# Performance work log

Measured on AMD Instinct MI355X. Metric: run time of the kernel, lower is better.

The kernel has to match this reference:

```python
import jax, jax.numpy as jnp
import numpy as np

N_NODES = 100000
N_EDGES = 1600000
N_GRAPHS = 1000
H = 128
F_IN = 128
F_EDGE = 16
DEPTH = 4


def setup_inputs() -> dict:
    key = jax.random.key(0)
    ks = jax.random.split(key, 10)
    s = 1.0 / np.sqrt(H)
    x = jax.random.normal(ks[0], (N_NODES, F_IN), dtype=jnp.float32)
    edge_index = jax.random.randint(ks[1], (2, N_EDGES), 0, N_NODES, dtype=jnp.int32)
    edge_attr = jax.random.normal(ks[2], (N_EDGES, F_EDGE), dtype=jnp.float32)
    batch = jnp.sort(jax.random.randint(ks[3], (N_NODES,), 0, N_GRAPHS, dtype=jnp.int32))
    W0 = jax.random.normal(ks[4], (F_IN, H), dtype=jnp.float32) * s
    b0 = jnp.zeros((H,), dtype=jnp.float32)
    W1 = jax.random.normal(ks[5], (DEPTH, H, H), dtype=jnp.float32) * s
    b1 = jnp.zeros((DEPTH, H), dtype=jnp.float32)
    W2 = jax.random.normal(ks[6], (DEPTH, H, H), dtype=jnp.float32) * s
    b2 = jnp.zeros((DEPTH, H), dtype=jnp.float32)
    Wf = jax.random.normal(ks[7], (H, 1), dtype=jnp.float32) * s
    bf = jnp.zeros((1,), dtype=jnp.float32)
    return {"x": x, "edge_index": edge_index, "edge_attr": edge_attr, "batch": batch,
            "W0": W0, "b0": b0, "W1": W1, "b1": b1, "W2": W2, "b2": b2, "Wf": Wf, "bf": bf}


def reference(x, edge_index, edge_attr, batch, W0, b0, W1, b1, W2, b2, Wf, bf):
    # edge_attr is read by the original forward but never used in the math.
    src, dst = edge_index[0], edge_index[1]
    n = x.shape[0]
    h0 = jax.nn.relu(x @ W0 + b0)  # [N, H]
    h = h0
    for i in range(DEPTH):
        # GINConv (eps=0): MLP(x + sum_{j in N(i)} x_j); messages flow src -> dst
        agg = jax.ops.segment_sum(h[src], dst, num_segments=n)  # [N, H]
        z = h + agg
        z = jax.nn.relu(z @ W1[i] + b1[i]) @ W2[i] + b2[i]
        # residual then relu (dropout p=0.02 is identity at eval)
        h = jax.nn.relu(z + h0)
    pooled = jax.ops.segment_sum(h, batch, num_segments=N_GRAPHS)  # [G, H]
    out = (pooled @ Wf + bf)[:, 0]  # [G]
    return out
```

## Files before the change

kernel.cpp:

```cpp
#include <hip/hip_runtime.h>

#define N_NODES 100000
#define N_EDGES 1600000
#define N_GRAPHS 1000
#define H 128
#define DEPTH 4
#define NB 391
#define BCAP 4864

typedef __attribute__((ext_vector_type(8))) short bf16x8;
typedef __attribute__((ext_vector_type(4))) float f32x4;

__device__ __forceinline__ unsigned short f2bf(float f) {
  unsigned int u = __float_as_uint(f);
  u += 0x7FFF + ((u >> 16) & 1);
  return (unsigned short)(u >> 16);
}
__device__ __forceinline__ float bflo(unsigned int v) { return __uint_as_float(v << 16); }
__device__ __forceinline__ float bfhi(unsigned int v) { return __uint_as_float(v & 0xFFFF0000u); }

__global__ __launch_bounds__(256) void k_bcnt(const int* __restrict__ dst, int* __restrict__ gcnt) {
  __shared__ int c[NB];
  int tid = threadIdx.x, e0 = blockIdx.x * 4096;
  for (int i = tid; i < NB; i += 256) c[i] = 0;
  __syncthreads();
#pragma unroll
  for (int i = 0; i < 16; ++i) {
    int e = e0 + i * 256 + tid;
    if (e < N_EDGES) atomicAdd(&c[dst[e] >> 8], 1);
  }
  __syncthreads();
  for (int i = tid; i < NB; i += 256)
    if (c[i]) atomicAdd(&gcnt[i], c[i]);
}

__global__ __launch_bounds__(512) void k_bscan(const int* __restrict__ gcnt, int* __restrict__ boff,
                                               int* __restrict__ cursor) {
  __shared__ int sh[512];
  int t = threadIdx.x;
  int v = (t < NB) ? gcnt[t] : 0;
  sh[t] = v;
  __syncthreads();
  for (int s = 1; s < 512; s <<= 1) {
    int x = (t >= s) ? sh[t - s] : 0;
    __syncthreads();
    sh[t] += x;
    __syncthreads();
  }
  if (t < NB) {
    int e = sh[t] - v;
    boff[t] = e;
    cursor[t] = e;
  }
  if (t == 0) boff[NB] = N_EDGES;
}

__global__ __launch_bounds__(256) void k_bucket(const int* __restrict__ src, const int* __restrict__ dst,
                                                int* __restrict__ cursor, unsigned int* __restrict__ ebuf) {
  __shared__ int cnt[NB];
  __shared__ int base[NB];
  int tid = threadIdx.x;
  int e0 = blockIdx.x * 4096;
  for (int i = tid; i < NB; i += 256) cnt[i] = 0;
  __syncthreads();
  unsigned int pk[16];
  int bk[16], rk[16];
#pragma unroll
  for (int i = 0; i < 16; ++i) {
    int e = e0 + i * 256 + tid;
    if (e < N_EDGES) {
      int s = src[e], d = dst[e];
      bk[i] = d >> 8;
      pk[i] = ((unsigned int)(d & 255) << 17) | (unsigned int)s;
      rk[i] = atomicAdd(&cnt[bk[i]], 1);
    } else
      bk[i] = -1;
  }
  __syncthreads();
  for (int i = tid; i < NB; i += 256)
    base[i] = cnt[i] ? atomicAdd(&cursor[i], cnt[i]) : 0;
  __syncthreads();
#pragma unroll
  for (int i = 0; i < 16; ++i)
    if (bk[i] >= 0) ebuf[base[bk[i]] + rk[i]] = pk[i];
}

__global__ __launch_bounds__(256) void k_bsort(const unsigned int* __restrict__ ebuf,
                                               const int* __restrict__ boff,
                                               int* __restrict__ csr, int* __restrict__ offs) {
  __shared__ unsigned int arr[BCAP];
  __shared__ unsigned int srt[BCAP];
  __shared__ unsigned short rnk[BCAP];
  __shared__ int cnt[256];
  __shared__ int off[257];
  int b = blockIdx.x, tid = threadIdx.x;
  int beg = boff[b], end = boff[b + 1];
  int ce = min(end - beg, BCAP);
  cnt[tid] = 0;
  __syncthreads();
  for (int i = tid; i < ce; i += 256) {
    unsigned int p = ebuf[beg + i];
    arr[i] = p;
    rnk[i] = (unsigned short)atomicAdd(&cnt[p >> 17], 1);
  }
  __syncthreads();
  int v = cnt[tid];
  off[tid + 1] = v;
  if (tid == 0) off[0] = 0;
  __syncthreads();
  for (int s = 1; s < 256; s <<= 1) {
    int x = (tid + 1 > s) ? off[tid + 1 - s] : 0;
    __syncthreads();
    off[tid + 1] += x;
    __syncthreads();
  }
  for (int i = tid; i < ce; i += 256) {
    unsigned int p = arr[i];
    srt[off[p >> 17] + rnk[i]] = p & 0x1FFFF;
  }
  __syncthreads();
  for (int i = tid; i < ce; i += 256) csr[beg + i] = (int)srt[i];
  int node = (b << 8) + tid;
  if (node < N_NODES) offs[node] = beg + off[tid];
  if (b == NB - 1 && tid == 0) offs[N_NODES] = N_EDGES;
}

__device__ __forceinline__ void stage_w(const float* __restrict__ Wg, unsigned short* Wt, int tid) {
  for (int idx = tid; idx < 2048; idx += 256) {
    int ng4 = idx & 31, kp = idx >> 5;
    float4 r0 = *(const float4*)&Wg[(2 * kp) * H + 4 * ng4];
    float4 r1 = *(const float4*)&Wg[(2 * kp + 1) * H + 4 * ng4];
    unsigned int p0 = (unsigned int)f2bf(r0.x) | ((unsigned int)f2bf(r1.x) << 16);
    unsigned int p1 = (unsigned int)f2bf(r0.y) | ((unsigned int)f2bf(r1.y) << 16);
    unsigned int p2 = (unsigned int)f2bf(r0.z) | ((unsigned int)f2bf(r1.z) << 16);
    unsigned int p3 = (unsigned int)f2bf(r0.w) | ((unsigned int)f2bf(r1.w) << 16);
    *(unsigned int*)&Wt[(4 * ng4 + 0) * 136 + 2 * kp] = p0;
    *(unsigned int*)&Wt[(4 * ng4 + 1) * 136 + 2 * kp] = p1;
    *(unsigned int*)&Wt[(4 * ng4 + 2) * 136 + 2 * kp] = p2;
    *(unsigned int*)&Wt[(4 * ng4 + 3) * 136 + 2 * kp] = p3;
  }
}

__global__ __launch_bounds__(256) void k_lin(const float* __restrict__ in, const float* __restrict__ Wg,
                                             const float* __restrict__ bg, unsigned short* __restrict__ outp) {
  __shared__ unsigned short Wt[128 * 136];
  __shared__ unsigned short zs[64 * 136];
  int tid = threadIdx.x;
  int lane = tid & 63, w = tid >> 6;
  int q = lane >> 4, l16 = lane & 15;
  int n0 = blockIdx.x * 64;

  stage_w(Wg, Wt, tid);

  int row = n0 + w * 16 + l16;
  int rr = (row < N_NODES) ? row : 0;
  bf16x8 afrag[4];
#pragma unroll
  for (int ks = 0; ks < 4; ++ks) {
    const float* p = &in[(size_t)rr * H + ks * 32 + q * 8];
    float4 f0 = *(const float4*)p;
    float4 f1 = *(const float4*)(p + 4);
    bf16x8 a;
    a[0] = (short)f2bf(f0.x); a[1] = (short)f2bf(f0.y); a[2] = (short)f2bf(f0.z); a[3] = (short)f2bf(f0.w);
    a[4] = (short)f2bf(f1.x); a[5] = (short)f2bf(f1.y); a[6] = (short)f2bf(f1.z); a[7] = (short)f2bf(f1.w);
    afrag[ks] = a;
  }
  f32x4 acc[8];
#pragma unroll
  for (int ct = 0; ct < 8; ++ct) acc[ct] = (f32x4){0.f, 0.f, 0.f, 0.f};
  __syncthreads();
#pragma unroll
  for (int ct = 0; ct < 8; ++ct)
#pragma unroll
    for (int ks = 0; ks < 4; ++ks) {
      bf16x8 b = *(bf16x8*)&Wt[(ct * 16 + l16) * 136 + ks * 32 + q * 8];
      acc[ct] = __builtin_amdgcn_mfma_f32_16x16x32_bf16(afrag[ks], b, acc[ct], 0, 0, 0);
    }
#pragma unroll
  for (int ct = 0; ct < 8; ++ct) {
    float bb = bg[ct * 16 + l16];
#pragma unroll
    for (int r = 0; r < 4; ++r) {
      float v = fmaxf(acc[ct][r] + bb, 0.f);
      zs[(w * 16 + q * 4 + r) * 136 + ct * 16 + l16] = f2bf(v);
    }
  }
  __syncthreads();
  int node = tid >> 2, cb = (tid & 3) * 32;
  if (n0 + node < N_NODES) {
#pragma unroll
    for (int i = 0; i < 4; ++i) {
      uint4 v = *(uint4*)&zs[node * 136 + cb + i * 8];
      *(uint4*)&outp[(size_t)(n0 + node) * H + cb + i * 8] = v;
    }
  }
}

__global__ __launch_bounds__(256) void k_agg(const unsigned short* __restrict__ hin, const int* __restrict__ offs,
                                             const int* __restrict__ csr, unsigned short* __restrict__ zin) {
  int node = blockIdx.x * 4 + (threadIdx.x >> 6);
  int lane = threadIdx.x & 63;
  if (node >= N_NODES) return;
  const unsigned int* hu = (const unsigned int*)hin;
  unsigned int self = hu[(size_t)node * 64 + lane];
  float sx = bflo(self), sy = bfhi(self);
  int beg = offs[node], end = offs[node + 1];
  for (int e = beg; e < end; e += 64) {
    int cnt = min(64, end - e);
    int idx = (lane < cnt) ? csr[e + lane] : 0;
    int j = 0;
    for (; j + 4 <= cnt; j += 4) {
      int s0 = __shfl(idx, j), s1 = __shfl(idx, j + 1), s2 = __shfl(idx, j + 2), s3 = __shfl(idx, j + 3);
      unsigned int v0 = hu[(size_t)s0 * 64 + lane];
      unsigned int v1 = hu[(size_t)s1 * 64 + lane];
      unsigned int v2 = hu[(size_t)s2 * 64 + lane];
      unsigned int v3 = hu[(size_t)s3 * 64 + lane];
      sx += bflo(v0); sy += bfhi(v0);
      sx += bflo(v1); sy += bfhi(v1);
      sx += bflo(v2); sy += bfhi(v2);
      sx += bflo(v3); sy += bfhi(v3);
    }
    for (; j < cnt; ++j) {
      int s = __shfl(idx, j);
      unsigned int v = hu[(size_t)s * 64 + lane];
      sx += bflo(v); sy += bfhi(v);
    }
  }
  unsigned int o = (unsigned int)f2bf(sx) | ((unsigned int)f2bf(sy) << 16);
  ((unsigned int*)zin)[(size_t)node * 64 + lane] = o;
}

__global__ __launch_bounds__(256) void k_mlp(const unsigned short* __restrict__ zin,
                                             const float* __restrict__ W1g, const float* __restrict__ b1g,
                                             const float* __restrict__ W2g, const float* __restrict__ b2g,
                                             const unsigned short* __restrict__ h0, unsigned short* __restrict__ h) {
  __shared__ unsigned short Wt[128 * 136];
  __shared__ unsigned short zs[64 * 136];
  int tid = threadIdx.x;
  int lane = tid & 63, w = tid >> 6;
  int q = lane >> 4, l16 = lane & 15;
  int n0 = blockIdx.x * 64;

  stage_w(W1g, Wt, tid);

  int row = n0 + w * 16 + l16;
  int rr = (row < N_NODES) ? row : 0;
  bf16x8 afrag[4];
#pragma unroll
  for (int ks = 0; ks < 4; ++ks)
    afrag[ks] = *(bf16x8*)&zin[(size_t)rr * H + ks * 32 + q * 8];

  f32x4 acc[8];
#pragma unroll
  for (int ct = 0; ct < 8; ++ct) acc[ct] = (f32x4){0.f, 0.f, 0.f, 0.f};
  __syncthreads();
#pragma unroll
  for (int ct = 0; ct < 8; ++ct)
#pragma unroll
    for (int ks = 0; ks < 4; ++ks) {
      bf16x8 b = *(bf16x8*)&Wt[(ct * 16 + l16) * 136 + ks * 32 + q * 8];
      acc[ct] = __builtin_amdgcn_mfma_f32_16x16x32_bf16(afrag[ks], b, acc[ct], 0, 0, 0);
    }
  __syncthreads();
  stage_w(W2g, Wt, tid);
#pragma unroll
  for (int ct = 0; ct < 8; ++ct) {
    float bb = b1g[ct * 16 + l16];
#pragma unroll
    for (int r = 0; r < 4; ++r) {
      float v = fmaxf(acc[ct][r] + bb, 0.f);
      zs[(w * 16 + q * 4 + r) * 136 + ct * 16 + l16] = f2bf(v);
    }
  }
  __syncthreads();
  bf16x8 a2[4];
#pragma unroll
  for (int ks = 0; ks < 4; ++ks)
    a2[ks] = *(bf16x8*)&zs[(w * 16 + l16) * 136 + ks * 32 + q * 8];
  f32x4 acc2[8];
#pragma unroll
  for (int ct = 0; ct < 8; ++ct) acc2[ct] = (f32x4){0.f, 0.f, 0.f, 0.f};
#pragma unroll
  for (int ct = 0; ct < 8; ++ct)
#pragma unroll
    for (int ks = 0; ks < 4; ++ks) {
      bf16x8 b = *(bf16x8*)&Wt[(ct * 16 + l16) * 136 + ks * 32 + q * 8];
      acc2[ct] = __builtin_amdgcn_mfma_f32_16x16x32_bf16(a2[ks], b, acc2[ct], 0, 0, 0);
    }
#pragma unroll
  for (int ct = 0; ct < 8; ++ct) {
    float bb = b2g[ct * 16 + l16];
#pragma unroll
    for (int r = 0; r < 4; ++r) {
      float v = acc2[ct][r] + bb;
      zs[(w * 16 + q * 4 + r) * 136 + ct * 16 + l16] = f2bf(v);
    }
  }
  __syncthreads();
  int node = tid >> 2, cb = (tid & 3) * 32;
  if (n0 + node < N_NODES) {
    size_t base = (size_t)(n0 + node) * H + cb;
#pragma unroll
    for (int i = 0; i < 4; ++i) {
      uint4 zv = *(uint4*)&zs[node * 136 + cb + i * 8];
      uint4 hv = *(const uint4*)&h0[base + i * 8];
      unsigned int zr[4] = {zv.x, zv.y, zv.z, zv.w};
      unsigned int hr[4] = {hv.x, hv.y, hv.z, hv.w};
      uint4 o;
      unsigned int orr[4];
#pragma unroll
      for (int j = 0; j < 4; ++j) {
        float a = fmaxf(bflo(zr[j]) + bflo(hr[j]), 0.f);
        float b = fmaxf(bfhi(zr[j]) + bfhi(hr[j]), 0.f);
        orr[j] = (unsigned int)f2bf(a) | ((unsigned int)f2bf(b) << 16);
      }
      o.x = orr[0]; o.y = orr[1]; o.z = orr[2]; o.w = orr[3];
      *(uint4*)&h[base + i * 8] = o;
    }
  }
}

__global__ void k_starts(const int* __restrict__ batch, int* __restrict__ starts) {
  int n = blockIdx.x * 256 + threadIdx.x;
  if (n >= N_NODES) return;
  int b = batch[n];
  if (n == 0) {
    for (int g = 0; g <= b; ++g) starts[g] = 0;
  } else {
    int bp = batch[n - 1];
    for (int g = bp + 1; g <= b; ++g) starts[g] = n;
  }
  if (n == N_NODES - 1) {
    for (int g = b + 1; g <= N_GRAPHS; ++g) starts[g] = N_NODES;
  }
}

__global__ __launch_bounds__(256) void k_pool(const unsigned short* __restrict__ h, const int* __restrict__ starts,
                                              const float* __restrict__ Wf, const float* __restrict__ bf_,
                                              float* __restrict__ out) {
  __shared__ float r[4];
  int g = blockIdx.x, tid = threadIdx.x;
  int lane = tid & 63, w = tid >> 6;
  int beg = starts[g], end = starts[g + 1];
  const unsigned int* hu = (const unsigned int*)h;
  float sx = 0.f, sy = 0.f;
  for (int n = beg + w; n < end; n += 4) {
    unsigned int v = hu[(size_t)n * 64 + lane];
    sx += bflo(v);
    sy += bfhi(v);
  }
  float val = sx * Wf[2 * lane] + sy * Wf[2 * lane + 1];
#pragma unroll
  for (int off = 32; off > 0; off >>= 1) val += __shfl_down(val, off);
  if (lane == 0) r[w] = val;
  __syncthreads();
  if (tid == 0) out[g] = r[0] + r[1] + r[2] + r[3] + bf_[0];
}

extern "C" void kernel_launch(void* const* d_in, const int* in_sizes, int n_in,
                              void* d_out, int out_size, void* d_ws, size_t ws_size,
                              hipStream_t stream) {
  const float* x = (const float*)d_in[0];
  const int* ei = (const int*)d_in[1];
  const int* srcv = ei;
  const int* dstv = ei + N_EDGES;
  const int* batch = (const int*)d_in[3];
  const float* W0 = (const float*)d_in[4];
  const float* b0 = (const float*)d_in[5];
  const float* W1 = (const float*)d_in[6];
  const float* b1 = (const float*)d_in[7];
  const float* W2 = (const float*)d_in[8];
  const float* b2 = (const float*)d_in[9];
  const float* Wf = (const float*)d_in[10];
  const float* bf_ = (const float*)d_in[11];
  float* out = (float*)d_out;

  char* ws = (char*)d_ws;
  size_t o = 0;
  auto alloc = [&](size_t bytes) {
    size_t r = o;
    o = (o + bytes + 255) & ~(size_t)255;
    return r;
  };
  int* offs = (int*)(ws + alloc((N_NODES + 1) * sizeof(int)));
  int* gcnt = (int*)(ws + alloc(NB * sizeof(int)));
  int* boff = (int*)(ws + alloc((NB + 1) * sizeof(int)));
  int* cursor = (int*)(ws + alloc(NB * sizeof(int)));
  unsigned int* ebuf = (unsigned int*)(ws + alloc((size_t)N_EDGES * 4));
  int* csr = (int*)(ws + alloc((size_t)N_EDGES * sizeof(int)));
  int* starts = (int*)(ws + alloc((N_GRAPHS + 1) * sizeof(int)));
  unsigned short* h0 = (unsigned short*)(ws + alloc((size_t)N_NODES * H * 2));
  unsigned short* h = (unsigned short*)(ws + alloc((size_t)N_NODES * H * 2));
  unsigned short* zin = (unsigned short*)(ws + alloc((size_t)N_NODES * H * 2));

  hipMemsetAsync(gcnt, 0, NB * sizeof(int), stream);
  k_bcnt<<<NB, 256, 0, stream>>>(dstv, gcnt);
  k_bscan<<<1, 512, 0, stream>>>(gcnt, boff, cursor);
  k_bucket<<<NB, 256, 0, stream>>>(srcv, dstv, cursor, ebuf);
  k_bsort<<<NB, 256, 0, stream>>>(ebuf, boff, csr, offs);
  k_starts<<<(N_NODES + 255) / 256, 256, 0, stream>>>(batch, starts);

  const int nblk = (N_NODES + 63) / 64;
  k_lin<<<nblk, 256, 0, stream>>>(x, W0, b0, h0);
  for (int i = 0; i < DEPTH; ++i) {
    const unsigned short* hin = (i == 0) ? h0 : h;
    k_agg<<<N_NODES / 4, 256, 0, stream>>>(hin, offs, csr, zin);
    k_mlp<<<nblk, 256, 0, stream>>>(zin, W1 + (size_t)i * H * H, b1 + (size_t)i * H,
                                    W2 + (size_t)i * H * H, b2 + (size_t)i * H, h0, h);
  }
  k_pool<<<N_GRAPHS, 256, 0, stream>>>(h, starts, Wf, bf_, out);
}
```

Before: 678.3 us.

## Fuse neighbor aggregation into MLP kernel with ping-pong h buffers

```diff
diff --git a/kernel.cpp b/kernel.cpp
--- a/kernel.cpp
+++ b/kernel.cpp
@@ -196,44 +196,12 @@
   }
 }
 
-__global__ __launch_bounds__(256) void k_agg(const unsigned short* __restrict__ hin, const int* __restrict__ offs,
-                                             const int* __restrict__ csr, unsigned short* __restrict__ zin) {
-  int node = blockIdx.x * 4 + (threadIdx.x >> 6);
-  int lane = threadIdx.x & 63;
-  if (node >= N_NODES) return;
-  const unsigned int* hu = (const unsigned int*)hin;
-  unsigned int self = hu[(size_t)node * 64 + lane];
-  float sx = bflo(self), sy = bfhi(self);
-  int beg = offs[node], end = offs[node + 1];
-  for (int e = beg; e < end; e += 64) {
-    int cnt = min(64, end - e);
-    int idx = (lane < cnt) ? csr[e + lane] : 0;
-    int j = 0;
-    for (; j + 4 <= cnt; j += 4) {
-      int s0 = __shfl(idx, j), s1 = __shfl(idx, j + 1), s2 = __shfl(idx, j + 2), s3 = __shfl(idx, j + 3);
-      unsigned int v0 = hu[(size_t)s0 * 64 + lane];
-      unsigned int v1 = hu[(size_t)s1 * 64 + lane];
-      unsigned int v2 = hu[(size_t)s2 * 64 + lane];
-      unsigned int v3 = hu[(size_t)s3 * 64 + lane];
-      sx += bflo(v0); sy += bfhi(v0);
-      sx += bflo(v1); sy += bfhi(v1);
-      sx += bflo(v2); sy += bfhi(v2);
-      sx += bflo(v3); sy += bfhi(v3);
-    }
-    for (; j < cnt; ++j) {
-      int s = __shfl(idx, j);
-      unsigned int v = hu[(size_t)s * 64 + lane];
-      sx += bflo(v); sy += bfhi(v);
-    }
-  }
-  unsigned int o = (unsigned int)f2bf(sx) | ((unsigned int)f2bf(sy) << 16);
-  ((unsigned int*)zin)[(size_t)node * 64 + lane] = o;
-}
-
-__global__ __launch_bounds__(256) void k_mlp(const unsigned short* __restrict__ zin,
-                                             const float* __restrict__ W1g, const float* __restrict__ b1g,
-                                             const float* __restrict__ W2g, const float* __restrict__ b2g,
-                                             const unsigned short* __restrict__ h0, unsigned short* __restrict__ h) {
+__global__ __launch_bounds__(256) void k_agg_mlp(const unsigned short* __restrict__ hin,
+                                                 const int* __restrict__ offs, const int* __restrict__ csr,
+                                                 const float* __restrict__ W1g, const float* __restrict__ b1g,
+                                                 const float* __restrict__ W2g, const float* __restrict__ b2g,
+                                                 const unsigned short* __restrict__ h0,
+                                                 unsigned short* __restrict__ hout) {
   __shared__ unsigned short Wt[128 * 136];
   __shared__ unsigned short zs[64 * 136];
   int tid = threadIdx.x;
@@ -243,12 +211,62 @@
 
   stage_w(W1g, Wt, tid);
 
-  int row = n0 + w * 16 + l16;
-  int rr = (row < N_NODES) ? row : 0;
+  const unsigned int* hu = (const unsigned int*)hin;
+  for (int m = 0; m < 16; ++m) {
+    int node = n0 + w * 16 + m;
+    if (node < N_NODES) {
+      unsigned int self = hu[(size_t)node * 64 + lane];
+      float sx = bflo(self), sy = bfhi(self);
+      int beg = offs[node], end = offs[node + 1];
+      for (int e = beg; e < end; e += 64) {
+        int cnt = min(64, end - e);
+        int idx = (lane < cnt) ? csr[e + lane] : 0;
+        int j = 0;
+        for (; j + 8 <= cnt; j += 8) {
+          int s0 = __shfl(idx, j), s1 = __shfl(idx, j + 1), s2 = __shfl(idx, j + 2), s3 = __shfl(idx, j + 3);
+          int s4 = __shfl(idx, j + 4), s5 = __shfl(idx, j + 5), s6 = __shfl(idx, j + 6), s7 = __shfl(idx, j + 7);
+          unsigned int v0 = hu[(size_t)s0 * 64 + lane];
+          unsigned int v1 = hu[(size_t)s1 * 64 + lane];
+          unsigned int v2 = hu[(size_t)s2 * 64 + lane];
+          unsigned int v3 = hu[(size_t)s3 * 64 + lane];
+          unsigned int v4 = hu[(size_t)s4 * 64 + lane];
+          unsigned int v5 = hu[(size_t)s5 * 64 + lane];
+          unsigned int v6 = hu[(size_t)s6 * 64 + lane];
+          unsigned int v7 = hu[(size_t)s7 * 64 + lane];
+          sx += bflo(v0); sy += bfhi(v0);
+          sx += bflo(v1); sy += bfhi(v1);
+          sx += bflo(v2); sy += bfhi(v2);
+          sx += bflo(v3); sy += bfhi(v3);
+          sx += bflo(v4); sy += bfhi(v4);
+          sx += bflo(v5); sy += bfhi(v5);
+          sx += bflo(v6); sy += bfhi(v6);
+          sx += bflo(v7); sy += bfhi(v7);
+        }
+        for (; j + 4 <= cnt; j += 4) {
+          int s0 = __shfl(idx, j), s1 = __shfl(idx, j + 1), s2 = __shfl(idx, j + 2), s3 = __shfl(idx, j + 3);
+          unsigned int v0 = hu[(size_t)s0 * 64 + lane];
+          unsigned int v1 = hu[(size_t)s1 * 64 + lane];
+          unsigned int v2 = hu[(size_t)s2 * 64 + lane];
+          unsigned int v3 = hu[(size_t)s3 * 64 + lane];
+          sx += bflo(v0); sy += bfhi(v0);
+          sx += bflo(v1); sy += bfhi(v1);
+          sx += bflo(v2); sy += bfhi(v2);
+          sx += bflo(v3); sy += bfhi(v3);
+        }
+        for (; j < cnt; ++j) {
+          int s = __shfl(idx, j);
+          unsigned int v = hu[(size_t)s * 64 + lane];
+          sx += bflo(v); sy += bfhi(v);
+        }
+      }
+      unsigned int o = (unsigned int)f2bf(sx) | ((unsigned int)f2bf(sy) << 16);
+      *(unsigned int*)&zs[(w * 16 + m) * 136 + 2 * lane] = o;
+    }
+  }
   bf16x8 afrag[4];
 #pragma unroll
   for (int ks = 0; ks < 4; ++ks)
-    afrag[ks] = *(bf16x8*)&zin[(size_t)rr * H + ks * 32 + q * 8];
+    afrag[ks] = *(bf16x8*)&zs[(w * 16 + l16) * 136 + ks * 32 + q * 8];
 
   f32x4 acc[8];
 #pragma unroll
@@ -315,7 +333,7 @@
         orr[j] = (unsigned int)f2bf(a) | ((unsigned int)f2bf(b) << 16);
       }
       o.x = orr[0]; o.y = orr[1]; o.z = orr[2]; o.w = orr[3];
-      *(uint4*)&h[base + i * 8] = o;
+      *(uint4*)&hout[base + i * 8] = o;
     }
   }
 }
@@ -390,8 +408,8 @@
   int* csr = (int*)(ws + alloc((size_t)N_EDGES * sizeof(int)));
   int* starts = (int*)(ws + alloc((N_GRAPHS + 1) * sizeof(int)));
   unsigned short* h0 = (unsigned short*)(ws + alloc((size_t)N_NODES * H * 2));
-  unsigned short* h = (unsigned short*)(ws + alloc((size_t)N_NODES * H * 2));
-  unsigned short* zin = (unsigned short*)(ws + alloc((size_t)N_NODES * H * 2));
+  unsigned short* hA = (unsigned short*)(ws + alloc((size_t)N_NODES * H * 2));
+  unsigned short* hB = (unsigned short*)(ws + alloc((size_t)N_NODES * H * 2));
 
   hipMemsetAsync(gcnt, 0, NB * sizeof(int), stream);
   k_bcnt<<<NB, 256, 0, stream>>>(dstv, gcnt);
@@ -402,11 +420,14 @@
 
   const int nblk = (N_NODES + 63) / 64;
   k_lin<<<nblk, 256, 0, stream>>>(x, W0, b0, h0);
+  const unsigned short* hin = h0;
+  unsigned short* houts[2] = {hA, hB};
   for (int i = 0; i < DEPTH; ++i) {
-    const unsigned short* hin = (i == 0) ? h0 : h;
-    k_agg<<<N_NODES / 4, 256, 0, stream>>>(hin, offs, csr, zin);
-    k_mlp<<<nblk, 256, 0, stream>>>(zin, W1 + (size_t)i * H * H, b1 + (size_t)i * H,
-                                    W2 + (size_t)i * H * H, b2 + (size_t)i * H, h0, h);
-  }
-  k_pool<<<N_GRAPHS, 256, 0, stream>>>(h, starts, Wf, bf_, out);
-}
+    unsigned short* hout = houts[i & 1];
+    k_agg_mlp<<<nblk, 256, 0, stream>>>(hin, offs, csr,
+                                        W1 + (size_t)i * H * H, b1 + (size_t)i * H,
+                                        W2 + (size_t)i * H * H, b2 + (size_t)i * H, h0, hout);
+    hin = hout;
+  }
+  k_pool<<<N_GRAPHS, 256, 0, stream>>>(hin, starts, Wf, bf_, out);
+}
```

Measured after the change: 842.4 us. +24.2%, slower.

## Store node features in 16-column slices so gather aggregation stays cache-resident

Applied to the files above, without the earlier changes.

```diff
diff --git a/kernel.cpp b/kernel.cpp
--- a/kernel.cpp
+++ b/kernel.cpp
@@ -7,6 +7,7 @@
 #define DEPTH 4
 #define NB 391
 #define BCAP 4864
+#define P16 ((size_t)N_NODES * 16)
 
 typedef __attribute__((ext_vector_type(8))) short bf16x8;
 typedef __attribute__((ext_vector_type(4))) float f32x4;
@@ -142,7 +143,7 @@
 }
 
 __global__ __launch_bounds__(256) void k_lin(const float* __restrict__ in, const float* __restrict__ Wg,
-                                             const float* __restrict__ bg, unsigned short* __restrict__ outp) {
+                                             const float* __restrict__ bg, unsigned short* __restrict__ outb) {
   __shared__ unsigned short Wt[128 * 136];
   __shared__ unsigned short zs[64 * 136];
   int tid = threadIdx.x;
@@ -186,54 +187,68 @@
     }
   }
   __syncthreads();
-  int node = tid >> 2, cb = (tid & 3) * 32;
-  if (n0 + node < N_NODES) {
+  int node = tid >> 2, q4 = tid & 3;
+  int gn = n0 + node;
+  if (gn < N_NODES) {
 #pragma unroll
     for (int i = 0; i < 4; ++i) {
-      uint4 v = *(uint4*)&zs[node * 136 + cb + i * 8];
-      *(uint4*)&outp[(size_t)(n0 + node) * H + cb + i * 8] = v;
-    }
-  }
-}
-
-__global__ __launch_bounds__(256) void k_agg(const unsigned short* __restrict__ hin, const int* __restrict__ offs,
-                                             const int* __restrict__ csr, unsigned short* __restrict__ zin) {
-  int node = blockIdx.x * 4 + (threadIdx.x >> 6);
-  int lane = threadIdx.x & 63;
-  if (node >= N_NODES) return;
-  const unsigned int* hu = (const unsigned int*)hin;
-  unsigned int self = hu[(size_t)node * 64 + lane];
-  float sx = bflo(self), sy = bfhi(self);
-  int beg = offs[node], end = offs[node + 1];
-  for (int e = beg; e < end; e += 64) {
-    int cnt = min(64, end - e);
-    int idx = (lane < cnt) ? csr[e + lane] : 0;
-    int j = 0;
-    for (; j + 4 <= cnt; j += 4) {
-      int s0 = __shfl(idx, j), s1 = __shfl(idx, j + 1), s2 = __shfl(idx, j + 2), s3 = __shfl(idx, j + 3);
-      unsigned int v0 = hu[(size_t)s0 * 64 + lane];
-      unsigned int v1 = hu[(size_t)s1 * 64 + lane];
-      unsigned int v2 = hu[(size_t)s2 * 64 + lane];
-      unsigned int v3 = hu[(size_t)s3 * 64 + lane];
-      sx += bflo(v0); sy += bfhi(v0);
-      sx += bflo(v1); sy += bfhi(v1);
-      sx += bflo(v2); sy += bfhi(v2);
-      sx += bflo(v3); sy += bfhi(v3);
-    }
-    for (; j < cnt; ++j) {
-      int s = __shfl(idx, j);
-      unsigned int v = hu[(size_t)s * 64 + lane];
-      sx += bflo(v); sy += bfhi(v);
-    }
-  }
-  unsigned int o = (unsigned int)f2bf(sx) | ((unsigned int)f2bf(sy) << 16);
-  ((unsigned int*)zin)[(size_t)node * 64 + lane] = o;
-}
-
-__global__ __launch_bounds__(256) void k_mlp(const unsigned short* __restrict__ zin,
+      uint4 v = *(uint4*)&zs[node * 136 + q4 * 32 + i * 8];
+      int cb = q4 * 2 + (i >> 1);
+      *(uint4*)&outb[(size_t)cb * P16 + (size_t)gn * 16 + (i & 1) * 8] = v;
+    }
+  }
+}
+
+__global__ __launch_bounds__(256) void k_agg(const unsigned short* __restrict__ hin_b,
+                                             const int* __restrict__ offs, const int* __restrict__ csr,
+                                             unsigned short* __restrict__ zin_b) {
+  int slice = blockIdx.x & 7;
+  int tile = blockIdx.x >> 3;
+  int w = threadIdx.x >> 6, l = threadIdx.x & 63;
+  int g = l >> 3, wd = l & 7;
+  const unsigned int* hbs = (const unsigned int*)(hin_b + (size_t)slice * P16);
+  unsigned int* zbs = (unsigned int*)(zin_b + (size_t)slice * P16);
+  int nbase = tile * 64 + w * 16;
+  int oidx = nbase + ((l <= 16) ? l : 16);
+  if (oidx > N_NODES) oidx = N_NODES;
+  int off_l = offs[oidx];
+#pragma unroll 1
+  for (int m = 0; m < 16; ++m) {
+    int n = nbase + m;
+    if (n >= N_NODES) break;
+    int beg = __shfl(off_l, m);
+    int end = __shfl(off_l, m + 1);
+    float ax = 0.f, ay = 0.f;
+    int e = beg + g;
+    for (; e + 8 < end; e += 16) {
+      int s0 = __builtin_nontemporal_load(&csr[e]);
+      int s1 = __builtin_nontemporal_load(&csr[e + 8]);
+      unsigned int v0 = hbs[(size_t)s0 * 8 + wd];
+      unsigned int v1 = hbs[(size_t)s1 * 8 + wd];
+      ax += bflo(v0); ay += bfhi(v0);
+      ax += bflo(v1); ay += bfhi(v1);
+    }
+    if (e < end) {
+      int s = __builtin_nontemporal_load(&csr[e]);
+      unsigned int v = hbs[(size_t)s * 8 + wd];
+      ax += bflo(v); ay += bfhi(v);
+    }
+    ax += __shfl_xor(ax, 8);  ay += __shfl_xor(ay, 8);
+    ax += __shfl_xor(ax, 16); ay += __shfl_xor(ay, 16);
+    ax += __shfl_xor(ax, 32); ay += __shfl_xor(ay, 32);
+    if (g == 0) {
+      unsigned int sv = hbs[(size_t)n * 8 + wd];
+      ax += bflo(sv); ay += bfhi(sv);
+      unsigned int o = (unsigned int)f2bf(ax) | ((unsigned int)f2bf(ay) << 16);
+      __builtin_nontemporal_store(o, &zbs[(size_t)n * 8 + wd]);
+    }
+  }
+}
+
+__global__ __launch_bounds__(256) void k_mlp(const unsigned short* __restrict__ zin_b,
                                              const float* __restrict__ W1g, const float* __restrict__ b1g,
                                              const float* __restrict__ W2g, const float* __restrict__ b2g,
-                                             const unsigned short* __restrict__ h0, unsigned short* __restrict__ h) {
+                                             const unsigned short* __restrict__ h0b, unsigned short* __restrict__ hb) {
   __shared__ unsigned short Wt[128 * 136];
   __shared__ unsigned short zs[64 * 136];
   int tid = threadIdx.x;
@@ -247,8 +262,10 @@
   int rr = (row < N_NODES) ? row : 0;
   bf16x8 afrag[4];
 #pragma unroll
-  for (int ks = 0; ks < 4; ++ks)
-    afrag[ks] = *(bf16x8*)&zin[(size_t)rr * H + ks * 32 + q * 8];
+  for (int ks = 0; ks < 4; ++ks) {
+    int cb = 2 * ks + (q >> 1);
+    afrag[ks] = *(bf16x8*)&zin_b[(size_t)cb * P16 + (size_t)rr * 16 + (q & 1) * 8];
+  }
 
   f32x4 acc[8];
 #pragma unroll
@@ -297,16 +314,17 @@
     }
   }
   __syncthreads();
-  int node = tid >> 2, cb = (tid & 3) * 32;
-  if (n0 + node < N_NODES) {
-    size_t base = (size_t)(n0 + node) * H + cb;
+  int node = tid >> 2, q4 = tid & 3;
+  int gn = n0 + node;
+  if (gn < N_NODES) {
 #pragma unroll
     for (int i = 0; i < 4; ++i) {
-      uint4 zv = *(uint4*)&zs[node * 136 + cb + i * 8];
-      uint4 hv = *(const uint4*)&h0[base + i * 8];
+      int cb = q4 * 2 + (i >> 1);
+      size_t gaddr = (size_t)cb * P16 + (size_t)gn * 16 + (i & 1) * 8;
+      uint4 zv = *(uint4*)&zs[node * 136 + q4 * 32 + i * 8];
+      uint4 hv = *(const uint4*)&h0b[gaddr];
       unsigned int zr[4] = {zv.x, zv.y, zv.z, zv.w};
       unsigned int hr[4] = {hv.x, hv.y, hv.z, hv.w};
-      uint4 o;
       unsigned int orr[4];
 #pragma unroll
       for (int j = 0; j < 4; ++j) {
@@ -314,8 +332,9 @@
         float b = fmaxf(bfhi(zr[j]) + bfhi(hr[j]), 0.f);
         orr[j] = (unsigned int)f2bf(a) | ((unsigned int)f2bf(b) << 16);
       }
+      uint4 o;
       o.x = orr[0]; o.y = orr[1]; o.z = orr[2]; o.w = orr[3];
-      *(uint4*)&h[base + i * 8] = o;
+      *(uint4*)&hb[gaddr] = o;
     }
   }
 }
@@ -335,17 +354,18 @@
   }
 }
 
-__global__ __launch_bounds__(256) void k_pool(const unsigned short* __restrict__ h, const int* __restrict__ starts,
+__global__ __launch_bounds__(256) void k_pool(const unsigned short* __restrict__ hb, const int* __restrict__ starts,
                                               const float* __restrict__ Wf, const float* __restrict__ bf_,
                                               float* __restrict__ out) {
   __shared__ float r[4];
   int g = blockIdx.x, tid = threadIdx.x;
   int lane = tid & 63, w = tid >> 6;
+  int cb = lane >> 3, wd = lane & 7;
   int beg = starts[g], end = starts[g + 1];
-  const unsigned int* hu = (const unsigned int*)h;
+  const unsigned int* hu = (const unsigned int*)(hb + (size_t)cb * P16);
   float sx = 0.f, sy = 0.f;
   for (int n = beg + w; n < end; n += 4) {
-    unsigned int v = hu[(size_t)n * 64 + lane];
+    unsigned int v = hu[(size_t)n * 8 + wd];
     sx += bflo(v);
     sy += bfhi(v);
   }
@@ -401,10 +421,11 @@
   k_starts<<<(N_NODES + 255) / 256, 256, 0, stream>>>(batch, starts);
 
   const int nblk = (N_NODES + 63) / 64;
+  const int nagg = 8 * ((N_NODES + 63) / 64);
   k_lin<<<nblk, 256, 0, stream>>>(x, W0, b0, h0);
   for (int i = 0; i < DEPTH; ++i) {
     const unsigned short* hin = (i == 0) ? h0 : h;
-    k_agg<<<N_NODES / 4, 256, 0, stream>>>(hin, offs, csr, zin);
+    k_agg<<<nagg, 256, 0, stream>>>(hin, offs, csr, zin);
     k_mlp<<<nblk, 256, 0, stream>>>(zin, W1 + (size_t)i * H * H, b1 + (size_t)i * H,
                                     W2 + (size_t)i * H * H, b2 + (size_t)i * H, h0, h);
   }
```

Result: slower. 1.502 ms (+121.4%).
